# Performance work log

Measured on AMD Instinct MI355X. Metric: run time of the kernel, lower is better.

## Reference

```python
import jax, jax.numpy as jnp
import numpy as np

K_HARD = 32
K_RAND = 32
SCALE_MAX = 100.0
NEG_FILL = -10000.0
EPS = 1e-12


def _normalize(x):
    return x / jnp.maximum(jnp.linalg.norm(x, axis=1, keepdims=True), EPS)


def _dir_loss(sim, scale, key):
    # One direction of InfoNCE with hard topk negatives + random negatives.
    B = sim.shape[0]
    diag = jnp.eye(B, dtype=bool)
    pos = jnp.diagonal(sim)                       # [B] positives
    sim_neg = jnp.where(diag, NEG_FILL, sim)      # mask self-similarity
    # hard negatives: per-row topk over masked sims (hard_ratio = 1.0)
    hard_vals, hard_idx = jax.lax.top_k(sim_neg, K_HARD)
    # valid pool for random negatives: not diagonal, not already a hard neg
    valid = (~diag).at[jnp.arange(B)[:, None], hard_idx].set(False)
    # uniform sampling without replacement via random-score top_k (fully on-device,
    # replaces the per-row nonzero/randperm loop); B-1-K_HARD >> min_valid_negs here
    r = jnp.where(valid, jax.random.uniform(key, (B, B)), -1.0)
    _, pick = jax.lax.top_k(r, K_RAND)
    rand_vals = jnp.take_along_axis(sim, pick, axis=1)  # picks exclude diag -> sim == sim_neg
    # logits: [pos | hard | rand], target class 0, scaled cross-entropy
    logits = jnp.concatenate([pos[:, None], hard_vals, rand_vals], axis=1) * scale
    return -jnp.mean(jax.nn.log_softmax(logits, axis=1)[:, 0])


def reference(h_img, h_txt, logit_scale):
    a = _normalize(h_img)
    b = _normalize(h_txt)
    sim = a @ b.T                                 # [B, B]
    scale = jnp.minimum(jnp.exp(logit_scale[0]), SCALE_MAX)
    k1, k2 = jax.random.split(jax.random.key(42))
    loss_i2t = _dir_loss(sim, scale, k1)
    loss_t2i = _dir_loss(sim.T, scale, k2)
    return 0.5 * (loss_i2t + loss_t2i)


def setup_inputs() -> dict:
    key = jax.random.key(0)
    k1, k2 = jax.random.split(key)
    B, D = 8192, 1024
    h_img = jax.random.normal(k1, (B, D), dtype=jnp.float32)
    h_txt = jax.random.normal(k2, (B, D), dtype=jnp.float32)
    logit_scale = jnp.full((1,), np.log(1.0 / 0.07), dtype=jnp.float32)
    return {"h_img": h_img, "h_txt": h_txt, "logit_scale": logit_scale}
```

## Files before the change

### kernel.cpp

```cpp
#include <hip/hip_runtime.h>
#include <hip/hip_bf16.h>


#define BN8 8192
#define DK 1024
#define KH 32
#define KR 32
#define LDSZ 132096

typedef __attribute__((ext_vector_type(4))) float f32x4;
typedef __attribute__((ext_vector_type(8))) int i32x8;
typedef __attribute__((ext_vector_type(4))) int i32x4;

#if __has_builtin(__builtin_amdgcn_exp2f)
#define EXP2(x) __builtin_amdgcn_exp2f(x)
#else
#define EXP2(x) exp2f(x)
#endif

static __device__ __forceinline__ unsigned f2bf(float f) {
  unsigned u = __float_as_uint(f);
  u = u + 0x7FFFu + ((u >> 16) & 1u);
  return u >> 16;
}
static __device__ __forceinline__ float bf2f(unsigned short v) {
  return __uint_as_float(((unsigned)v) << 16);
}
static __device__ __forceinline__ float keyval(unsigned u) {
  unsigned short v = (u & 0x8000u) ? (unsigned short)(u ^ 0x8000u) : (unsigned short)(~u);
  return bf2f(v);
}

static __device__ __forceinline__ unsigned pk_skey(unsigned w) {
  const unsigned m = ((w >> 15) & 0x00010001u) * 0x7FFFu;
  return w ^ (m | 0x80008000u);
}
static __device__ __forceinline__ unsigned pkmax(unsigned a, unsigned b) {
  unsigned d; asm("v_pk_max_u16 %0, %1, %2" : "=v"(d) : "v"(a), "v"(b)); return d;
}
static __device__ __forceinline__ unsigned pkmin(unsigned a, unsigned b) {
  unsigned d; asm("v_pk_min_u16 %0, %1, %2" : "=v"(d) : "v"(a), "v"(b)); return d;
}
#define INS4P(K0, K1, K2, K3, U) do { unsigned _u = (U); \
    unsigned _n0 = pkmin(K0, _u); K0 = pkmax(K0, _u); \
    unsigned _n1 = pkmin(K1, _n0); K1 = pkmax(K1, _n0); \
    unsigned _n2 = pkmin(K2, _n1); K2 = pkmax(K2, _n1); \
    K3 = pkmax(K3, _n2); } while (0)

__global__ __launch_bounds__(256) void norm_convert8(const float* __restrict__ img,
                                                     const float* __restrict__ txt,
                                                     unsigned char* __restrict__ a8,
                                                     unsigned char* __restrict__ b8) {
  const int row = blockIdx.x;
  const int t = threadIdx.x;
  const float* src;
  unsigned char* dst;
  if (row < BN8) { src = img + (size_t)row * DK; dst = a8 + (size_t)row * DK; }
  else          { src = txt + (size_t)(row - BN8) * DK; dst = b8 + (size_t)(row - BN8) * DK; }
  float4 v = ((const float4*)src)[t];
  float ss = v.x * v.x + v.y * v.y + v.z * v.z + v.w * v.w;
  for (int off = 32; off; off >>= 1) ss += __shfl_xor(ss, off);
  __shared__ float red[4];
  if ((t & 63) == 0) red[t >> 6] = ss;
  __syncthreads();
  float tot = red[0] + red[1] + red[2] + red[3];
  float inv = 1.0f / fmaxf(sqrtf(tot), 1e-12f);
  const int p0 = __builtin_amdgcn_cvt_pk_fp8_f32(v.x * inv, v.y * inv, 0, false);
  const int p1 = __builtin_amdgcn_cvt_pk_fp8_f32(v.z * inv, v.w * inv, 0, false);
  ((unsigned*)dst)[t] = ((unsigned)p0 & 0xFFFFu) | ((unsigned)p1 << 16);
}

#define GLDS(SRC, DST) __builtin_amdgcn_global_load_lds( \
    (const __attribute__((address_space(1))) void*)(SRC), \
    (__attribute__((address_space(3))) void*)(DST), 16, 0, 0)

static __device__ __forceinline__ i32x8 pack8(const char* p0, const char* p1) {
  i32x4 lo = *(const i32x4*)p0;
  i32x4 hi = *(const i32x4*)p1;
  i32x8 r;
  r[0] = lo[0]; r[1] = lo[1]; r[2] = lo[2]; r[3] = lo[3];
  r[4] = hi[0]; r[5] = hi[1]; r[6] = hi[2]; r[7] = hi[3];
  return r;
}

__global__ __launch_bounds__(512, 2) void gemm_fused(const unsigned char* __restrict__ A,
                                                     const unsigned char* __restrict__ Bm,
                                                     const float* __restrict__ lsc,
                                                     float* __restrict__ posv,
                                                     unsigned* __restrict__ rowsK,
                                                     float* __restrict__ rowsE,
                                                     unsigned* __restrict__ colsK,
                                                     float* __restrict__ colsE) {
  extern __shared__ char lds[];
  float* esColL = (float*)(lds + 131072);
  const int t = threadIdx.x;
  const int lane = t & 63;
  const int w = t >> 6;
  const int wr = w >> 2, wc = w & 3;
  const int wch = wc >> 1, g4 = wr * 2 + (wc & 1);
  const int llo = lane & 15, lhi = lane >> 4;

  const int bid = blockIdx.y * 32 + blockIdx.x;
  const int swz = (bid & 7) * 128 + (bid >> 3);
  const int row0 = (swz >> 5) << 8;
  const int col0 = (swz & 31) << 8;

  if (t < 256) esColL[t] = 0.f;

  const int scol = (((lane & 7) ^ (lane >> 3)) << 4);
  const char* asg = (const char*)A +
      (size_t)(row0 + wr * 128 + wc * 8 + (lane >> 3)) * 1024 + scol;
  const char* bsg = (const char*)Bm +
      (size_t)(col0 + wch * 128 + g4 * 8 + (lane >> 3)) * 1024 + scol;
  const int ldsAo = wr * 16384 + wc * 1024;
  const int ldsBo = 32768 + wch * 16384 + g4 * 1024;

  const int sw0 = (((2 * lhi) ^ (llo & 7)) << 4);
  const int sw1 = sw0 ^ 16;
  const int abyte = wr * 16384 + llo * 128;
  const int bbyte = 32768 + wc * 8192 + llo * 128;

  f32x4 acc[8][4] = {};

  {
#pragma unroll
    for (int e = 0; e < 4; ++e) GLDS(bsg + e * 32768, lds + ldsBo + e * 4096);
#pragma unroll
    for (int e = 0; e < 4; ++e) GLDS(asg + e * 32768, lds + ldsAo + e * 4096);
    asm volatile("s_waitcnt vmcnt(0)" ::: "memory");
  }

  for (int u = 0; u < 8; ++u) {
    asm volatile("s_barrier" ::: "memory");
    const int cur = (u & 1) << 16;
    const int nxt = cur ^ 65536;
    if (u < 7) {
      const int kb = (u + 1) * 128;
#pragma unroll
      for (int e = 0; e < 4; ++e) GLDS(bsg + e * 32768 + kb, lds + nxt + ldsBo + e * 4096);
#pragma unroll
      for (int e = 0; e < 4; ++e) GLDS(asg + e * 32768 + kb, lds + nxt + ldsAo + e * 4096);
    }
    const char* cb = lds + cur;
    i32x8 bfr[4];
#pragma unroll
    for (int n = 0; n < 4; ++n)
      bfr[n] = pack8(cb + bbyte + n * 2048 + sw0, cb + bbyte + n * 2048 + sw1);
#pragma unroll
    for (int MQ = 0; MQ < 4; ++MQ) {
      i32x8 af[2];
#pragma unroll
      for (int j = 0; j < 2; ++j)
        af[j] = pack8(cb + abyte + (MQ * 2 + j) * 2048 + sw0,
                      cb + abyte + (MQ * 2 + j) * 2048 + sw1);
      __builtin_amdgcn_s_setprio(1);
#pragma unroll
      for (int j = 0; j < 2; ++j)
#pragma unroll
        for (int n = 0; n < 4; ++n)
          acc[MQ * 2 + j][n] = __builtin_amdgcn_mfma_scale_f32_16x16x128_f8f6f4(
              bfr[n], af[j], acc[MQ * 2 + j][n], 0, 0,
              0, 0x7F7F7F7F, 0, 0x7F7F7F7F);
      __builtin_amdgcn_s_setprio(0);
    }
    if (u < 7) asm volatile("s_waitcnt vmcnt(0)" ::: "memory");
  }

  asm volatile("s_waitcnt lgkmcnt(0)" ::: "memory");
  asm volatile("s_barrier" ::: "memory");
#pragma unroll
  for (int m = 0; m < 8; ++m) {
    const int R = wr * 128 + m * 16 + llo;
    const int key = (R & 7) << 1;
#pragma unroll
    for (int n = 0; n < 4; ++n) {
      const int g = wc * 16 + n * 4 + lhi;
      ushort4 pk;
      pk.x = (unsigned short)f2bf(acc[m][n][0]);
      pk.y = (unsigned short)f2bf(acc[m][n][1]);
      pk.z = (unsigned short)f2bf(acc[m][n][2]);
      pk.w = (unsigned short)f2bf(acc[m][n][3]);
      *(ushort4*)(lds + R * 512 + (g ^ key) * 8) = pk;
    }
  }
  asm volatile("s_waitcnt lgkmcnt(0)" ::: "memory");
  __syncthreads();

  const float s = fminf(__expf(lsc[0]), 100.0f);
  const float s2 = s * 1.44269504f;
  const float c2 = -s2;
  const int rp = row0 >> 8, cp = col0 >> 8;
  const bool dgb = (row0 == col0);

  {
    const int R = t >> 1;
    const int h = t & 1;
    const int Rg = row0 + R;
    const int key = (R & 7) << 1;
    unsigned K0 = 0, K1 = 0, K2 = 0, K3 = 0;
    float es = 0.f;
    for (int gg = 0; gg < 32; ++gg) {
      const int g = h * 32 + gg;
      const char* gbase = lds + R * 512 + ((g ^ key) * 8);
      unsigned w0 = *(const unsigned*)gbase;
      unsigned w1 = *(const unsigned*)(gbase + 4);
      unsigned k0 = pk_skey(w0), k1 = pk_skey(w1);
      float a0 = EXP2(fmaf(bf2f((unsigned short)(w0 & 0xFFFFu)), s2, c2));
      float a1 = EXP2(fmaf(bf2f((unsigned short)(w0 >> 16)), s2, c2));
      float b0 = EXP2(fmaf(bf2f((unsigned short)(w1 & 0xFFFFu)), s2, c2));
      float b1 = EXP2(fmaf(bf2f((unsigned short)(w1 >> 16)), s2, c2));
      if (dgb) {
        const unsigned d = (unsigned)(R - 4 * g);
        if (d < 4u) {
          if (d == 0)      { posv[Rg] = bf2f((unsigned short)(w0 & 0xFFFFu)); k0 &= 0xFFFF0000u; a0 = 0.f; }
          else if (d == 1) { posv[Rg] = bf2f((unsigned short)(w0 >> 16));     k0 &= 0x0000FFFFu; a1 = 0.f; }
          else if (d == 2) { posv[Rg] = bf2f((unsigned short)(w1 & 0xFFFFu)); k1 &= 0xFFFF0000u; b0 = 0.f; }
          else             { posv[Rg] = bf2f((unsigned short)(w1 >> 16));     k1 &= 0x0000FFFFu; b1 = 0.f; }
        }
      }
      INS4P(K0, K1, K2, K3, k0);
      INS4P(K0, K1, K2, K3, k1);
      es += (a0 + a1) + (b0 + b1);
    }
    const size_t rb = ((size_t)Rg * 32 + cp) * 8 + h * 4;
    rowsK[rb + 0] = K0; rowsK[rb + 1] = K1; rowsK[rb + 2] = K2; rowsK[rb + 3] = K3;
    es += __shfl_xor(es, 1);
    if (h == 0) rowsE[(size_t)Rg * 32 + cp] = es;
  }

  {
    const int p = t & 127;
    const int seg = t >> 7;
    const int gq = p >> 1;
    const int sub = (p & 1) * 4;
    unsigned K0 = 0, K1 = 0, K2 = 0, K3 = 0;
    float e0 = 0.f, e1 = 0.f;
    for (int rr = 0; rr < 64; ++rr) {
      const int R = seg * 64 + rr;
      const unsigned wv = *(const unsigned*)(lds + R * 512 +
                             ((gq ^ ((R & 7) << 1)) * 8) + sub);
      unsigned wk = pk_skey(wv);
      float elo = EXP2(fmaf(bf2f((unsigned short)(wv & 0xFFFFu)), s2, c2));
      float ehi = EXP2(fmaf(bf2f((unsigned short)(wv >> 16)), s2, c2));
      if (dgb) {
        if (R == 2 * p)     { wk &= 0xFFFF0000u; elo = 0.f; }
        if (R == 2 * p + 1) { wk &= 0x0000FFFFu; ehi = 0.f; }
      }
      INS4P(K0, K1, K2, K3, wk);
      e0 += elo; e1 += ehi;
    }
    atomicAdd(&esColL[2 * p], e0);
    atomicAdd(&esColL[2 * p + 1], e1);
    const size_t b0 = ((size_t)(col0 + 2 * p) * 32 + rp) * 8 + seg * 2;
    const size_t b1 = ((size_t)(col0 + 2 * p + 1) * 32 + rp) * 8 + seg * 2;
    colsK[b0 + 0] = ((K0 & 0xFFFFu) << 16) | (K1 & 0xFFFFu);
    colsK[b0 + 1] = ((K2 & 0xFFFFu) << 16) | (K3 & 0xFFFFu);
    colsK[b1 + 0] = (K0 & 0xFFFF0000u) | (K1 >> 16);
    colsK[b1 + 1] = (K2 & 0xFFFF0000u) | (K3 >> 16);
  }
  __syncthreads();
  if (t < 256) colsE[(size_t)(col0 + t) * 32 + rp] = esColL[t];
}

template <int NW>
static __device__ __forceinline__ void fin_core(const unsigned* __restrict__ kb,
                                                const float* __restrict__ eb,
                                                const float* __restrict__ posv, int i,
                                                float s, float* __restrict__ outp) {
  const int lane = threadIdx.x & 63;
  const float s2 = s * 1.44269504f, c2 = -s2;
  unsigned K[NW];
#pragma unroll
  for (int j = 0; j < NW / 4; ++j) {
    uint4 v = ((const uint4*)kb)[lane * (NW / 4) + j];
    K[j * 4 + 0] = v.x; K[j * 4 + 1] = v.y; K[j * 4 + 2] = v.z; K[j * 4 + 3] = v.w;
  }
  float es = (lane < 32) ? eb[lane] : 0.f;
  for (int off = 32; off; off >>= 1) es += __shfl_xor(es, off);
  const float pos = posv[i];

  unsigned mk = 0;
#pragma unroll
  for (int j = 0; j < NW; ++j) { unsigned a = K[j] >> 16; mk = a > mk ? a : mk; }
  for (int off = 32; off; off >>= 1) { unsigned o = __shfl_xor(mk, off); mk = o > mk ? o : mk; }

  auto cnt = [&](unsigned mid) {
    int c = 0;
#pragma unroll
    for (int j = 0; j < NW; ++j)
      c += (int)((K[j] >> 16) > mid) + (int)((K[j] & 0xFFFFu) > mid);
    for (int off = 32; off; off >>= 1) c += __shfl_xor(c, off);
    return c;
  };

  unsigned lo = mk > 576u ? mk - 576u : 0u, hi = mk;
  if (cnt(lo) < KH) lo = 0;
  while (lo < hi) {
    const unsigned mid = (lo + hi) >> 1;
    if (cnt(mid) <= KH - 1) hi = mid; else lo = mid + 1;
  }
  const unsigned T = lo;
  const int cab = cnt(T);

  float hs = 0.f;
#pragma unroll
  for (int j = 0; j < NW; ++j) {
    const unsigned a = K[j] >> 16, b = K[j] & 0xFFFFu;
    if (a > T) hs += EXP2(fmaf(keyval(a), s2, c2));
    if (b > T) hs += EXP2(fmaf(keyval(b), s2, c2));
  }
  for (int off = 32; off; off >>= 1) hs += __shfl_xor(hs, off);

  if (lane == 0) {
    const float hard = hs + (float)(KH - cab) * EXP2(fmaf(keyval(T), s2, c2));
    const float valid = fmaxf(es - hard, 0.f);
    const float rho = (float)KR / (float)(BN8 - 1 - KH);
    const float D = EXP2(fmaf(pos, s2, c2)) + hard + rho * valid;
    *outp = s + __logf(D) - s * pos;
  }
}

__global__ __launch_bounds__(256) void finalize_rc(const unsigned* __restrict__ rowsK,
                                                   const float* __restrict__ rowsE,
                                                   const unsigned* __restrict__ colsK,
                                                   const float* __restrict__ colsE,
                                                   const float* __restrict__ posv,
                                                   const float* __restrict__ lsc,
                                                   float* __restrict__ losses) {
  const int w = threadIdx.x >> 6;
  const float s = fminf(__expf(lsc[0]), 100.0f);
  if (blockIdx.x < 2048) {
    const int i = blockIdx.x * 4 + w;
    fin_core<4>(rowsK + (size_t)i * 256, rowsE + (size_t)i * 32, posv, i, s, &losses[i]);
  } else {
    const int i = (blockIdx.x - 2048) * 4 + w;
    fin_core<4>(colsK + (size_t)i * 256, colsE + (size_t)i * 32, posv, i, s,
                &losses[BN8 + i]);
  }
}

__global__ __launch_bounds__(256) void finalize(const float* __restrict__ losses,
                                                float* __restrict__ out) {
  float ssum = 0.f;
  for (int j = threadIdx.x; j < 2 * BN8; j += 256) ssum += losses[j];
  for (int off = 32; off; off >>= 1) ssum += __shfl_xor(ssum, off);
  __shared__ float red[4];
  if ((threadIdx.x & 63) == 0) red[threadIdx.x >> 6] = ssum;
  __syncthreads();
  if (threadIdx.x == 0)
    out[0] = (red[0] + red[1] + red[2] + red[3]) / (2.0f * BN8);
}

extern "C" void kernel_launch(void* const* d_in, const int* in_sizes, int n_in,
                              void* d_out, int out_size, void* d_ws, size_t ws_size,
                              hipStream_t stream) {
  const float* img = (const float*)d_in[0];
  const float* txt = (const float*)d_in[1];
  const float* lsc = (const float*)d_in[2];
  float* out = (float*)d_out;
  char* ws = (char*)d_ws;

  unsigned char* a8 = (unsigned char*)ws;
  unsigned char* b8 = (unsigned char*)(ws + ((size_t)8u << 20));
  unsigned* rowsK = (unsigned*)(ws + ((size_t)16u << 20));
  unsigned* colsK = (unsigned*)(ws + ((size_t)24u << 20));
  float* rowsE = (float*)(ws + ((size_t)32u << 20));
  float* colsE = (float*)(ws + ((size_t)33u << 20));
  float* posv = (float*)(ws + ((size_t)34u << 20));
  float* losses = (float*)(ws + ((size_t)34u << 20) + 65536);

  norm_convert8<<<2 * BN8, 256, 0, stream>>>(img, txt, a8, b8);

  gemm_fused<<<dim3(32, 32), 512, LDSZ, stream>>>(a8, b8, lsc, posv,
                                                  rowsK, rowsE, colsK, colsE);
  finalize_rc<<<4096, 256, 0, stream>>>(rowsK, rowsE, colsK, colsE, posv, lsc, losses);

  finalize<<<1, 256, 0, stream>>>(losses, out);
}
```

Before: 177.8 us.

## Store exponentials as bf16 keys in LDS and reuse them for column pass

The row pass now computes exp(s*(sim-1)) once per element, packs the truncated bf16 exponentials as the top-k sort keys (positive floats order like unsigned ints), and writes them back into LDS. The column pass then reads these precomputed exponentials instead of recomputing exp and the sign-flip keys, using a narrower 2-deep insertion per column from uint2 reads. Finalize sums key values directly rather than re-exponentiating. This removes duplicate transcendental work at the cost of an extra LDS write, a barrier, and truncating exp values to bf16, which changes tie behaviour and precision of the hard-negative set. Row reads are also rotated to spread LDS bank access.

Result: faster. 165.9 us, median of 2 (-6.7%).

```diff
diff --git a/kernel.cpp b/kernel.cpp
--- a/kernel.cpp
+++ b/kernel.cpp
@@ -26,15 +26,7 @@
 static __device__ __forceinline__ float bf2f(unsigned short v) {
   return __uint_as_float(((unsigned)v) << 16);
 }
-static __device__ __forceinline__ float keyval(unsigned u) {
-  unsigned short v = (u & 0x8000u) ? (unsigned short)(u ^ 0x8000u) : (unsigned short)(~u);
-  return bf2f(v);
-}
-
-static __device__ __forceinline__ unsigned pk_skey(unsigned w) {
-  const unsigned m = ((w >> 15) & 0x00010001u) * 0x7FFFu;
-  return w ^ (m | 0x80008000u);
-}
+
 static __device__ __forceinline__ unsigned pkmax(unsigned a, unsigned b) {
   unsigned d; asm("v_pk_max_u16 %0, %1, %2" : "=v"(d) : "v"(a), "v"(b)); return d;
 }
@@ -46,6 +38,9 @@
     unsigned _n1 = pkmin(K1, _n0); K1 = pkmax(K1, _n0); \
     unsigned _n2 = pkmin(K2, _n1); K2 = pkmax(K2, _n1); \
     K3 = pkmax(K3, _n2); } while (0)
+#define INS2P(K0, K1, U) do { unsigned _u = (U); \
+    unsigned _n0 = pkmin(K0, _u); K0 = pkmax(K0, _u); \
+    K1 = pkmax(K1, _n0); } while (0)
 
 __global__ __launch_bounds__(256) void norm_convert8(const float* __restrict__ img,
                                                      const float* __restrict__ txt,
@@ -197,83 +192,84 @@
     const int h = t & 1;
     const int Rg = row0 + R;
     const int key = (R & 7) << 1;
+    char* rowbase = lds + R * 512;
     unsigned K0 = 0, K1 = 0, K2 = 0, K3 = 0;
     float es = 0.f;
     for (int gg = 0; gg < 32; ++gg) {
-      const int g = h * 32 + gg;
-      const char* gbase = lds + R * 512 + ((g ^ key) * 8);
-      unsigned w0 = *(const unsigned*)gbase;
-      unsigned w1 = *(const unsigned*)(gbase + 4);
-      unsigned k0 = pk_skey(w0), k1 = pk_skey(w1);
-      float a0 = EXP2(fmaf(bf2f((unsigned short)(w0 & 0xFFFFu)), s2, c2));
-      float a1 = EXP2(fmaf(bf2f((unsigned short)(w0 >> 16)), s2, c2));
-      float b0 = EXP2(fmaf(bf2f((unsigned short)(w1 & 0xFFFFu)), s2, c2));
-      float b1 = EXP2(fmaf(bf2f((unsigned short)(w1 >> 16)), s2, c2));
+      const int q = h * 32 + ((gg + R) & 31);
+      uint2 wv = *(const uint2*)(rowbase + q * 8);
+      float e0 = EXP2(fmaf(bf2f((unsigned short)(wv.x & 0xFFFFu)), s2, c2));
+      float e1 = EXP2(fmaf(bf2f((unsigned short)(wv.x >> 16)), s2, c2));
+      float e2 = EXP2(fmaf(bf2f((unsigned short)(wv.y & 0xFFFFu)), s2, c2));
+      float e3 = EXP2(fmaf(bf2f((unsigned short)(wv.y >> 16)), s2, c2));
       if (dgb) {
+        const int g = q ^ key;
         const unsigned d = (unsigned)(R - 4 * g);
         if (d < 4u) {
-          if (d == 0)      { posv[Rg] = bf2f((unsigned short)(w0 & 0xFFFFu)); k0 &= 0xFFFF0000u; a0 = 0.f; }
-          else if (d == 1) { posv[Rg] = bf2f((unsigned short)(w0 >> 16));     k0 &= 0x0000FFFFu; a1 = 0.f; }
-          else if (d == 2) { posv[Rg] = bf2f((unsigned short)(w1 & 0xFFFFu)); k1 &= 0xFFFF0000u; b0 = 0.f; }
-          else             { posv[Rg] = bf2f((unsigned short)(w1 >> 16));     k1 &= 0x0000FFFFu; b1 = 0.f; }
+          const unsigned short v =
+              (d & 2) ? ((d & 1) ? (unsigned short)(wv.y >> 16) : (unsigned short)(wv.y & 0xFFFFu))
+                      : ((d & 1) ? (unsigned short)(wv.x >> 16) : (unsigned short)(wv.x & 0xFFFFu));
+          posv[Rg] = bf2f(v);
+          if (d == 0) e0 = 0.f; else if (d == 1) e1 = 0.f;
+          else if (d == 2) e2 = 0.f; else e3 = 0.f;
         }
       }
-      INS4P(K0, K1, K2, K3, k0);
-      INS4P(K0, K1, K2, K3, k1);
-      es += (a0 + a1) + (b0 + b1);
+      es += (e0 + e1) + (e2 + e3);
+      const unsigned p01 = (__float_as_uint(e0) >> 16) | (__float_as_uint(e1) & 0xFFFF0000u);
+      const unsigned p23 = (__float_as_uint(e2) >> 16) | (__float_as_uint(e3) & 0xFFFF0000u);
+      INS4P(K0, K1, K2, K3, p01);
+      INS4P(K0, K1, K2, K3, p23);
+      uint2 ov; ov.x = p01; ov.y = p23;
+      *(uint2*)(rowbase + q * 8) = ov;
     }
     const size_t rb = ((size_t)Rg * 32 + cp) * 8 + h * 4;
     rowsK[rb + 0] = K0; rowsK[rb + 1] = K1; rowsK[rb + 2] = K2; rowsK[rb + 3] = K3;
     es += __shfl_xor(es, 1);
     if (h == 0) rowsE[(size_t)Rg * 32 + cp] = es;
   }
+  asm volatile("s_waitcnt lgkmcnt(0)" ::: "memory");
+  __syncthreads();
 
   {
-    const int p = t & 127;
-    const int seg = t >> 7;
-    const int gq = p >> 1;
-    const int sub = (p & 1) * 4;
-    unsigned K0 = 0, K1 = 0, K2 = 0, K3 = 0;
-    float e0 = 0.f, e1 = 0.f;
-    for (int rr = 0; rr < 64; ++rr) {
-      const int R = seg * 64 + rr;
-      const unsigned wv = *(const unsigned*)(lds + R * 512 +
-                             ((gq ^ ((R & 7) << 1)) * 8) + sub);
-      unsigned wk = pk_skey(wv);
-      float elo = EXP2(fmaf(bf2f((unsigned short)(wv & 0xFFFFu)), s2, c2));
-      float ehi = EXP2(fmaf(bf2f((unsigned short)(wv >> 16)), s2, c2));
-      if (dgb) {
-        if (R == 2 * p)     { wk &= 0xFFFF0000u; elo = 0.f; }
-        if (R == 2 * p + 1) { wk &= 0x0000FFFFu; ehi = 0.f; }
-      }
-      INS4P(K0, K1, K2, K3, wk);
-      e0 += elo; e1 += ehi;
-    }
-    atomicAdd(&esColL[2 * p], e0);
-    atomicAdd(&esColL[2 * p + 1], e1);
-    const size_t b0 = ((size_t)(col0 + 2 * p) * 32 + rp) * 8 + seg * 2;
-    const size_t b1 = ((size_t)(col0 + 2 * p + 1) * 32 + rp) * 8 + seg * 2;
-    colsK[b0 + 0] = ((K0 & 0xFFFFu) << 16) | (K1 & 0xFFFFu);
-    colsK[b0 + 1] = ((K2 & 0xFFFFu) << 16) | (K3 & 0xFFFFu);
-    colsK[b1 + 0] = (K0 & 0xFFFF0000u) | (K1 >> 16);
-    colsK[b1 + 1] = (K2 & 0xFFFF0000u) | (K3 >> 16);
+    const int p2 = t & 63;
+    const int seg = t >> 6;
+    unsigned A0 = 0, A1 = 0, B0 = 0, B1 = 0;
+    float e0 = 0.f, e1 = 0.f, e2 = 0.f, e3 = 0.f;
+    for (int rr = 0; rr < 32; ++rr) {
+      const int R = seg * 32 + rr;
+      const int q = p2 ^ ((R & 7) << 1);
+      uint2 wv = *(const uint2*)(lds + R * 512 + q * 8);
+      INS2P(A0, A1, wv.x);
+      INS2P(B0, B1, wv.y);
+      e0 += __uint_as_float(wv.x << 16);
+      e1 += __uint_as_float(wv.x & 0xFFFF0000u);
+      e2 += __uint_as_float(wv.y << 16);
+      e3 += __uint_as_float(wv.y & 0xFFFF0000u);
+    }
+    const int cb = 4 * p2;
+    atomicAdd(&esColL[cb + 0], e0);
+    atomicAdd(&esColL[cb + 1], e1);
+    atomicAdd(&esColL[cb + 2], e2);
+    atomicAdd(&esColL[cb + 3], e3);
+    colsK[((size_t)(col0 + cb + 0) * 32 + rp) * 8 + seg] = ((A0 & 0xFFFFu) << 16) | (A1 & 0xFFFFu);
+    colsK[((size_t)(col0 + cb + 1) * 32 + rp) * 8 + seg] = (A0 & 0xFFFF0000u) | (A1 >> 16);
+    colsK[((size_t)(col0 + cb + 2) * 32 + rp) * 8 + seg] = ((B0 & 0xFFFFu) << 16) | (B1 & 0xFFFFu);
+    colsK[((size_t)(col0 + cb + 3) * 32 + rp) * 8 + seg] = (B0 & 0xFFFF0000u) | (B1 >> 16);
   }
   __syncthreads();
   if (t < 256) colsE[(size_t)(col0 + t) * 32 + rp] = esColL[t];
 }
 
-template <int NW>
 static __device__ __forceinline__ void fin_core(const unsigned* __restrict__ kb,
                                                 const float* __restrict__ eb,
                                                 const float* __restrict__ posv, int i,
                                                 float s, float* __restrict__ outp) {
   const int lane = threadIdx.x & 63;
   const float s2 = s * 1.44269504f, c2 = -s2;
-  unsigned K[NW];
-#pragma unroll
-  for (int j = 0; j < NW / 4; ++j) {
-    uint4 v = ((const uint4*)kb)[lane * (NW / 4) + j];
-    K[j * 4 + 0] = v.x; K[j * 4 + 1] = v.y; K[j * 4 + 2] = v.z; K[j * 4 + 3] = v.w;
+  unsigned K[4];
+  {
+    uint4 v = ((const uint4*)kb)[lane];
+    K[0] = v.x; K[1] = v.y; K[2] = v.z; K[3] = v.w;
   }
   float es = (lane < 32) ? eb[lane] : 0.f;
   for (int off = 32; off; off >>= 1) es += __shfl_xor(es, off);
@@ -281,13 +277,13 @@
 
   unsigned mk = 0;
 #pragma unroll
-  for (int j = 0; j < NW; ++j) { unsigned a = K[j] >> 16; mk = a > mk ? a : mk; }
+  for (int j = 0; j < 4; ++j) { unsigned a = K[j] >> 16; mk = a > mk ? a : mk; }
   for (int off = 32; off; off >>= 1) { unsigned o = __shfl_xor(mk, off); mk = o > mk ? o : mk; }
 
   auto cnt = [&](unsigned mid) {
     int c = 0;
 #pragma unroll
-    for (int j = 0; j < NW; ++j)
+    for (int j = 0; j < 4; ++j)
       c += (int)((K[j] >> 16) > mid) + (int)((K[j] & 0xFFFFu) > mid);
     for (int off = 32; off; off >>= 1) c += __shfl_xor(c, off);
     return c;
@@ -304,15 +300,15 @@
 
   float hs = 0.f;
 #pragma unroll
-  for (int j = 0; j < NW; ++j) {
+  for (int j = 0; j < 4; ++j) {
     const unsigned a = K[j] >> 16, b = K[j] & 0xFFFFu;
-    if (a > T) hs += EXP2(fmaf(keyval(a), s2, c2));
-    if (b > T) hs += EXP2(fmaf(keyval(b), s2, c2));
+    if (a > T) hs += __uint_as_float(a << 16);
+    if (b > T) hs += __uint_as_float(b << 16);
   }
   for (int off = 32; off; off >>= 1) hs += __shfl_xor(hs, off);
 
   if (lane == 0) {
-    const float hard = hs + (float)(KH - cab) * EXP2(fmaf(keyval(T), s2, c2));
+    const float hard = hs + (float)(KH - cab) * __uint_as_float(T << 16);
     const float valid = fmaxf(es - hard, 0.f);
     const float rho = (float)KR / (float)(BN8 - 1 - KH);
     const float D = EXP2(fmaf(pos, s2, c2)) + hard + rho * valid;
@@ -331,11 +327,11 @@
   const float s = fminf(__expf(lsc[0]), 100.0f);
   if (blockIdx.x < 2048) {
     const int i = blockIdx.x * 4 + w;
-    fin_core<4>(rowsK + (size_t)i * 256, rowsE + (size_t)i * 32, posv, i, s, &losses[i]);
+    fin_core(rowsK + (size_t)i * 256, rowsE + (size_t)i * 32, posv, i, s, &losses[i]);
   } else {
     const int i = (blockIdx.x - 2048) * 4 + w;
-    fin_core<4>(colsK + (size_t)i * 256, colsE + (size_t)i * 32, posv, i, s,
-                &losses[BN8 + i]);
+    fin_core(colsK + (size_t)i * 256, colsE + (size_t)i * 32, posv, i, s,
+             &losses[BN8 + i]);
   }
 }
 
```
